# Optimization experiments

Hardware: AMD Instinct MI355X
Metric: run time of the kernel (lower is better)

The kernel has to match this reference:

```python
import jax, jax.numpy as jnp
import numpy as np
import math

NSAMPLE = 16
ATTN_TEMP = 1.0
LEAKY = 0.1
BN_EPS = 1e-5


def _knn(k, query, ref):
    # query [B,Nq,3], ref [B,Nr,3] -> idx [B,Nq,k] (indices into ref, nearest first)
    d = (jnp.sum(query * query, -1)[:, :, None]
         + jnp.sum(ref * ref, -1)[:, None, :]
         - 2.0 * jnp.einsum('bqc,brc->bqr', query, ref))
    _, idx = jax.lax.top_k(-d, k)
    return idx


def _gather(pts, idx):
    # pts [B,N,C], idx [B,M,K] -> [B,M,K,C]
    return jax.vmap(lambda p, i: p[i])(pts, idx)


def _bn_eval(x, g, b):
    # eval-mode BatchNorm2d with running_mean=0, running_var=1
    return x * (g / jnp.sqrt(1.0 + BN_EPS)) + b


def _leaky(x):
    return jnp.where(x >= 0, x, LEAKY * x)


def setup_inputs() -> dict:
    key = jax.random.key(0)
    ks = jax.random.split(key, 25)
    B, N, D, Cm, H = 2, 4096, 64, 64, 8
    f = jax.random.normal
    inp = {
        'xyz1': f(ks[0], (B, 3, N), jnp.float32),
        'xyz2': f(ks[1], (B, 3, N), jnp.float32),
        'xyz2w': f(ks[2], (B, 3, N), jnp.float32),
        'points1': f(ks[3], (B, D, N), jnp.float32),
        'points2': f(ks[4], (B, D, N), jnp.float32),
        'mlp_W0': f(ks[5], (Cm, 2 * D + 3), jnp.float32) * 0.1,
        'mlp_b0': f(ks[6], (Cm,), jnp.float32) * 0.05,
        'mlp_W1': f(ks[7], (Cm, Cm), jnp.float32) * 0.1,
        'mlp_b1': f(ks[8], (Cm,), jnp.float32) * 0.05,
        'wn_W0': f(ks[9], (H, 3), jnp.float32) * 0.3,
        'wn_b0': f(ks[10], (H,), jnp.float32) * 0.05,
        'wn_g0': jax.random.uniform(ks[11], (H,), jnp.float32, 0.5, 1.5),
        'wn_be0': f(ks[12], (H,), jnp.float32) * 0.05,
        'wn_W1': f(ks[13], (H, H), jnp.float32) * 0.3,
        'wn_b1': f(ks[14], (H,), jnp.float32) * 0.05,
        'wn_g1': jax.random.uniform(ks[15], (H,), jnp.float32, 0.5, 1.5),
        'wn_be1': f(ks[16], (H,), jnp.float32) * 0.05,
        'wn_W2': f(ks[17], (Cm, H), jnp.float32) * 0.3,
        'wn_b2': f(ks[18], (Cm,), jnp.float32) * 0.05,
        'wn_g2': jax.random.uniform(ks[19], (Cm,), jnp.float32, 0.5, 1.5),
        'wn_be2': f(ks[20], (Cm,), jnp.float32) * 0.05,
    }
    return inp


def reference(xyz1, xyz2, xyz2w, points1, points2,
              mlp_W0, mlp_b0, mlp_W1, mlp_b1,
              wn_W0, wn_b0, wn_g0, wn_be0,
              wn_W1, wn_b1, wn_g1, wn_be1,
              wn_W2, wn_b2, wn_g2, wn_be2):
    K = NSAMPLE
    B, C, N1 = xyz1.shape  # C == 3
    p1 = xyz1.transpose(0, 2, 1)    # [B,N1,3]
    p2 = xyz2.transpose(0, 2, 1)
    p2w = xyz2w.transpose(0, 2, 1)
    f1 = points1.transpose(0, 2, 1)  # [B,N1,D]
    f2 = points2.transpose(0, 2, 1)

    def mlp(f):
        f = _leaky(jnp.einsum('bnkc,oc->bnko', f, mlp_W0) + mlp_b0)
        f = _leaky(jnp.einsum('bnkc,oc->bnko', f, mlp_W1) + mlp_b1)
        return f

    idx = _knn(K, p1, p2)
    dir_xyz = _gather(p2, idx) - p1[:, :, None, :]          # [B,N1,K,3]
    idxw = _knn(K, p1, p2w)
    dir_xyzw = _gather(p2w, idxw) - p1[:, :, None, :]

    g1 = jnp.broadcast_to(f1[:, :, None, :], (B, N1, K, f1.shape[-1]))
    feat = mlp(jnp.concatenate([g1, _gather(f2, idx), dir_xyz], -1))    # [B,N1,K,Cm]
    featw = mlp(jnp.concatenate([g1, _gather(f2, idxw), dir_xyzw], -1))  # [B,N1,K,Cm]

    # per-channel K x K attention, contracted over all N1 points
    wqk = jnp.einsum('bnkc,bnlc->bckl', feat, featw)        # [B,Cm,K,K]
    wqk = jnp.clip(jax.nn.softmax(wqk / ATTN_TEMP, -1) / math.sqrt(C), 1e-10)
    # sum over trailing K is pushed into the attention matrix (same math)
    costw = jnp.einsum('bnlc,bcl->bcn', featw, wqk.sum(-1))  # [B,Cm,N1]
    cost = jnp.einsum('bnlc,bcl->bcn', feat, wqk.sum(-2))    # [B,Cm,N1]

    # self-neighborhood aggregation with WeightNet (bn=True, eval mode)
    idx_s = _knn(K, p1, p1)
    dir_s = _gather(p1, idx_s) - p1[:, :, None, :]           # [B,N1,K,3]
    h = jax.nn.relu(_bn_eval(jnp.einsum('bnkc,oc->bnko', dir_s, wn_W0) + wn_b0, wn_g0, wn_be0))
    h = jax.nn.relu(_bn_eval(jnp.einsum('bnkc,oc->bnko', h, wn_W1) + wn_b1, wn_g1, wn_be1))
    w = jax.nn.relu(_bn_eval(jnp.einsum('bnkc,oc->bnko', h, wn_W2) + wn_b2, wn_g2, wn_be2))  # [B,N1,K,Cm]

    grouped = _gather(cost.transpose(0, 2, 1), idx_s) + _gather(costw.transpose(0, 2, 1), idx_s)  # [B,N1,K,Cm]
    return jnp.einsum('bnkc,bnkc->bcn', w, grouped)          # [B,Cm,N1]
```

## Files before the change

### kernel.cpp

```cpp
#include <hip/hip_runtime.h>
#include <math.h>

#define B_  2
#define N_  4096
#define K_  16
#define D_  64
#define CM_ 64
#define H_  8

#define NSEG  8
#define SEGSZ (N_ / NSEG)
#define QPB   256
#define LIM   16
#define BATCH 8
#define TAUS  512

__device__ __forceinline__ void ce64(unsigned long long& a, unsigned long long& b) {
    bool sw = b < a;
    unsigned long long lo = sw ? b : a;
    unsigned long long hi = sw ? a : b;
    a = lo; b = hi;
}
__device__ __forceinline__ void cef(float& a, float& b) {
    float lo = fminf(a, b), hi = fmaxf(a, b);
    a = lo; b = hi;
}

#define SORT16_(e, CE) do { \
    CE(e[0],e[1]); CE(e[2],e[3]); CE(e[4],e[5]); CE(e[6],e[7]); \
    CE(e[8],e[9]); CE(e[10],e[11]); CE(e[12],e[13]); CE(e[14],e[15]); \
    CE(e[0],e[2]); CE(e[1],e[3]); CE(e[4],e[6]); CE(e[5],e[7]); \
    CE(e[8],e[10]); CE(e[9],e[11]); CE(e[12],e[14]); CE(e[13],e[15]); \
    CE(e[1],e[2]); CE(e[5],e[6]); CE(e[9],e[10]); CE(e[13],e[14]); \
    CE(e[0],e[4]); CE(e[1],e[5]); CE(e[2],e[6]); CE(e[3],e[7]); \
    CE(e[8],e[12]); CE(e[9],e[13]); CE(e[10],e[14]); CE(e[11],e[15]); \
    CE(e[2],e[4]); CE(e[3],e[5]); CE(e[10],e[12]); CE(e[11],e[13]); \
    CE(e[1],e[2]); CE(e[3],e[4]); CE(e[5],e[6]); \
    CE(e[9],e[10]); CE(e[11],e[12]); CE(e[13],e[14]); \
    CE(e[0],e[8]); CE(e[1],e[9]); CE(e[2],e[10]); CE(e[3],e[11]); \
    CE(e[4],e[12]); CE(e[5],e[13]); CE(e[6],e[14]); CE(e[7],e[15]); \
    CE(e[4],e[8]); CE(e[5],e[9]); CE(e[6],e[10]); CE(e[7],e[11]); \
    CE(e[2],e[4]); CE(e[3],e[5]); CE(e[6],e[8]); CE(e[7],e[9]); \
    CE(e[10],e[12]); CE(e[11],e[13]); \
    CE(e[1],e[2]); CE(e[3],e[4]); CE(e[5],e[6]); CE(e[7],e[8]); \
    CE(e[9],e[10]); CE(e[11],e[12]); CE(e[13],e[14]); \
} while (0)

#define BMERGE16_(d, CE) do { \
    CE(d[0],d[8]); CE(d[1],d[9]); CE(d[2],d[10]); CE(d[3],d[11]); \
    CE(d[4],d[12]); CE(d[5],d[13]); CE(d[6],d[14]); CE(d[7],d[15]); \
    CE(d[0],d[4]); CE(d[1],d[5]); CE(d[2],d[6]); CE(d[3],d[7]); \
    CE(d[8],d[12]); CE(d[9],d[13]); CE(d[10],d[14]); CE(d[11],d[15]); \
    CE(d[0],d[2]); CE(d[1],d[3]); CE(d[4],d[6]); CE(d[5],d[7]); \
    CE(d[8],d[10]); CE(d[9],d[11]); CE(d[12],d[14]); CE(d[13],d[15]); \
    CE(d[0],d[1]); CE(d[2],d[3]); CE(d[4],d[5]); CE(d[6],d[7]); \
    CE(d[8],d[9]); CE(d[10],d[11]); CE(d[12],d[13]); CE(d[14],d[15]); \
} while (0)

__global__ __launch_bounds__(256) void knn_tau_kernel(
    const float* __restrict__ xyz1, const float* __restrict__ xyz2,
    const float* __restrict__ xyz2w,
    float* __restrict__ tauBuf)
{
    const int b = blockIdx.y, which = blockIdx.z;
    const float* q = xyz1 + (size_t)b * 3 * N_;
    const float* r = (which == 0 ? xyz2 : (which == 1 ? xyz2w : xyz1)) + (size_t)b * 3 * N_;

    const int tid = threadIdx.x;
    const int qi = blockIdx.x * QPB + tid;
    const float qx = q[qi], qy = q[N_ + qi], qz = q[2 * N_ + qi];
    const float qq = qx * qx + qy * qy + qz * qz;

    __shared__ float4 tile[TAUS];
    __shared__ float  bufD[LIM * QPB];

    float bd[K_];
#pragma unroll
    for (int i = 0; i < K_; ++i) bd[i] = 3.4e38f;
    float tau = 3.4e38f;
    float c = 0.5f * (qq - tau);
    c -= fabsf(c) * 0.0009765625f + 1e-20f;
    int cnt = 0;

    for (int j = tid; j < TAUS; j += QPB) {
        float x = r[j], y = r[N_ + j], z = r[2 * N_ + j];
        tile[j] = make_float4(x, y, z, x * x + y * y + z * z);
    }
    __syncthreads();

    auto compactF = [&](int m_end) {
        float e[16];
#pragma unroll
        for (int m = 0; m < 16; ++m) {
            float dv = bufD[m * QPB + tid];
            e[m] = (m < m_end) ? dv : 3.4e38f;
        }
        SORT16_(e, cef);
#pragma unroll
        for (int i = 0; i < 16; ++i) bd[i] = fminf(bd[i], e[15 - i]);
        BMERGE16_(bd, cef);
        tau = fminf(tau, bd[K_ - 1]);
        c = 0.5f * (qq - tau);
        c -= fabsf(c) * 0.0009765625f + 1e-20f;
    };

    for (int j0 = 0; j0 < TAUS; j0 += BATCH) {
        float s8[BATCH], d8[BATCH];
#pragma unroll
        for (int u = 0; u < BATCH; ++u) {
            float4 t = tile[j0 + u];
            float dot = qx * t.x + qy * t.y + qz * t.z;
            s8[u] = dot - 0.5f * t.w;
            d8[u] = fmaxf((qq + t.w) - 2.0f * dot, 0.0f);
        }
#pragma unroll
        for (int u = 0; u < BATCH; ++u) {
            if (s8[u] > c) { bufD[cnt * QPB + tid] = d8[u]; ++cnt; }
        }
        if (__any(cnt > 8)) { compactF(cnt); cnt = 0; }
    }
    if (__any(cnt != 0)) compactF(cnt);

    tauBuf[((size_t)b * 3 + which) * N_ + qi] = bd[K_ - 1];
}

__global__ __launch_bounds__(256) void knn_seg_kernel(
    const float* __restrict__ xyz1, const float* __restrict__ xyz2,
    const float* __restrict__ xyz2w,
    const float* __restrict__ tauBuf,
    float* __restrict__ segD, int* __restrict__ segI)
{
    const int b = blockIdx.y;
    const int which = blockIdx.z >> 3;
    const int seg   = blockIdx.z & 7;
    const float* q = xyz1 + (size_t)b * 3 * N_;
    const float* r = (which == 0 ? xyz2 : (which == 1 ? xyz2w : xyz1)) + (size_t)b * 3 * N_;

    const int tid = threadIdx.x;
    const int qi = blockIdx.x * QPB + tid;
    const float qx = q[qi], qy = q[N_ + qi], qz = q[2 * N_ + qi];
    const float qq = qx * qx + qy * qy + qz * qz;

    __shared__ float4 tile[SEGSZ];
    __shared__ float  bufD[LIM * QPB];
    __shared__ int    bufI[LIM * QPB];

    unsigned long long bd[K_];
#pragma unroll
    for (int i = 0; i < K_; ++i) bd[i] = ~0ull;
    float tau = tauBuf[((size_t)b * 3 + which) * N_ + qi];
    float c = 0.5f * (qq - tau);
    c -= fabsf(c) * 0.0009765625f + 1e-20f;
    int cnt = 0;

    const int base0 = seg * SEGSZ;
    for (int j = tid; j < SEGSZ; j += QPB) {
        float x = r[base0 + j], y = r[N_ + base0 + j], z = r[2 * N_ + base0 + j];
        tile[j] = make_float4(x, y, z, x * x + y * y + z * z);
    }
    __syncthreads();

    auto compact = [&](int m_end) {
        unsigned long long e[16];
#pragma unroll
        for (int m = 0; m < 16; ++m) {
            float dv = bufD[m * QPB + tid];
            int   iv = bufI[m * QPB + tid];
            unsigned long long key =
                ((unsigned long long)__float_as_uint(dv) << 32) | (unsigned)iv;
            e[m] = (m < m_end) ? key : ~0ull;
        }
        SORT16_(e, ce64);
#pragma unroll
        for (int i = 0; i < 16; ++i) {
            unsigned long long cand = e[15 - i];
            if (cand < bd[i]) bd[i] = cand;
        }
        BMERGE16_(bd, ce64);
        tau = fminf(tau, __uint_as_float((unsigned)(bd[K_ - 1] >> 32)));
        c = 0.5f * (qq - tau);
        c -= fabsf(c) * 0.0009765625f + 1e-20f;
    };

    for (int j0 = 0; j0 < SEGSZ; j0 += BATCH) {
        float s8[BATCH], d8[BATCH];
#pragma unroll
        for (int u = 0; u < BATCH; ++u) {
            float4 t = tile[j0 + u];
            float dot = qx * t.x + qy * t.y + qz * t.z;
            s8[u] = dot - 0.5f * t.w;
            d8[u] = fmaxf((qq + t.w) - 2.0f * dot, 0.0f);
        }
#pragma unroll
        for (int u = 0; u < BATCH; ++u) {
            if (s8[u] > c) {
                bufD[cnt * QPB + tid] = d8[u];
                bufI[cnt * QPB + tid] = base0 + j0 + u;
                ++cnt;
            }
        }
        if (__any(cnt > 8)) { compact(cnt); cnt = 0; }
    }
    if (__any(cnt != 0)) compact(cnt);

    const size_t ob = ((((size_t)b * 3 + which) * NSEG + seg) * N_ + qi) * K_;
#pragma unroll
    for (int i = 0; i < K_; ++i) {
        segD[ob + i] = __uint_as_float((unsigned)(bd[i] >> 32));
        segI[ob + i] = (int)(unsigned)bd[i];
    }
}

__global__ __launch_bounds__(256) void knn_merge_kernel(
    const float* __restrict__ segD, const int* __restrict__ segI,
    int* __restrict__ idxA, int* __restrict__ idxB, int* __restrict__ idxS)
{
    const int b = blockIdx.y, which = blockIdx.z;
    const int qi = blockIdx.x * 256 + threadIdx.x;
    unsigned long long m[K_];
#pragma unroll
    for (int i = 0; i < K_; ++i) m[i] = ~0ull;
    for (int s = 0; s < NSEG; ++s) {
        const size_t ob = ((((size_t)b * 3 + which) * NSEG + s) * N_ + qi) * K_;
        for (int e = 0; e < K_; ++e) {
            unsigned long long key =
                ((unsigned long long)__float_as_uint(segD[ob + e]) << 32)
                | (unsigned)segI[ob + e];
            if (key >= m[K_ - 1]) break;
            m[K_ - 1] = key;
#pragma unroll
            for (int i = K_ - 1; i > 0; --i) {
                if (m[i] < m[i - 1]) {
                    unsigned long long t = m[i]; m[i] = m[i - 1]; m[i - 1] = t;
                }
            }
        }
    }
    int* outp = (which == 0 ? idxA : (which == 1 ? idxB : idxS));
    int* op = outp + ((size_t)b * N_ + qi) * K_;
#pragma unroll
    for (int i = 0; i < K_; ++i) op[i] = (int)(unsigned)m[i];
}

__global__ __launch_bounds__(256) void pre_gemm_kernel(
    const float* __restrict__ points1, const float* __restrict__ points2,
    const float* __restrict__ W0,
    float* __restrict__ G1, float* __restrict__ P2)
{
    const int b = blockIdx.y, which = blockIdx.z;
    const float* src = which ? points2 : points1;
    float* dst = which ? P2 : G1;
    const int woff = which ? 64 : 0;
    const int n0 = blockIdx.x * 64;
    const int tid = threadIdx.x;

    __shared__ float sW[64 * 65];
    __shared__ float sA[64 * 68];

    for (int i = tid; i < 4096; i += 256) {
        int c = i & 63, o = i >> 6;
        sW[c * 65 + o] = W0[o * 131 + woff + c];
    }
    for (int i = tid; i < 4096; i += 256) {
        int n = i & 63, c = i >> 6;
        sA[c * 68 + n] = src[((size_t)b * 64 + c) * N_ + n0 + n];
    }
    __syncthreads();

    const int o = tid & 63, qg = tid >> 6;
    float acc[16];
#pragma unroll
    for (int j = 0; j < 16; ++j) acc[j] = 0.f;
    for (int c = 0; c < 64; ++c) {
        float w = sW[c * 65 + o];
        const float4* ap = (const float4*)&sA[c * 68 + qg * 16];
#pragma unroll
        for (int m = 0; m < 4; ++m) {
            float4 a4 = ap[m];
            acc[4 * m + 0] += w * a4.x;
            acc[4 * m + 1] += w * a4.y;
            acc[4 * m + 2] += w * a4.z;
            acc[4 * m + 3] += w * a4.w;
        }
    }
#pragma unroll
    for (int j = 0; j < 16; ++j)
        dst[((size_t)b * N_ + n0 + qg * 16 + j) * 64 + o] = acc[j];
}

__global__ __launch_bounds__(256) void mlp2_kernel(
    const float* __restrict__ xyz1, const float* __restrict__ xyz2,
    const float* __restrict__ xyz2w,
    const int* __restrict__ idxA, const int* __restrict__ idxB,
    const float* __restrict__ G1, const float* __restrict__ P2,
    const float* __restrict__ W0, const float* __restrict__ b0,
    const float* __restrict__ W1, const float* __restrict__ b1,
    float* __restrict__ feat, float* __restrict__ featw)
{
    const int b = blockIdx.y, which = blockIdx.z;
    const int* idx = which ? idxB : idxA;
    const float* refxyz = (which ? xyz2w : xyz2) + (size_t)b * 3 * N_;
    float* outp = which ? featw : feat;
    const int n0 = blockIdx.x * 8;
    const int tid = threadIdx.x;
    const int w = tid >> 6, lane = tid & 63;

    __shared__ float sh0[64 * 132];
    __shared__ float sW1[64 * 68];
    __shared__ float sWc[3 * 64];
    __shared__ float sB0[64];
    __shared__ float sQ[3][8];
    __shared__ int   sIdx[128];

    for (int i = tid; i < 4096; i += 256) {
        int c = i & 63, o = i >> 6;
        sW1[c * 68 + o] = W1[o * 64 + c];
    }
    if (tid < 192) { int m = tid >> 6, o = tid & 63; sWc[m * 64 + o] = W0[o * 131 + 128 + m]; }
    if (tid < 64) sB0[tid] = b0[tid];
    if (tid < 24) { int m = tid >> 3, j = tid & 7; sQ[m][j] = xyz1[((size_t)b * 3 + m) * N_ + n0 + j]; }
    if (tid < 128) sIdx[tid] = idx[((size_t)b * N_ + n0 + (tid >> 4)) * K_ + (tid & 15)];
    __syncthreads();

    {
        const int o = lane;
        const float wc0 = sWc[o], wc1 = sWc[64 + o], wc2 = sWc[128 + o];
        const float bb0 = sB0[o];
#pragma unroll
        for (int p = 0; p < 2; ++p) {
            const int pl = w * 2 + p;
            const float g1 = G1[((size_t)b * N_ + n0 + pl) * 64 + o];
            const float qx = sQ[0][pl], qy = sQ[1][pl], qz = sQ[2][pl];
            for (int k = 0; k < K_; ++k) {
                const int row = pl * K_ + k;
                const int ii = sIdx[row];
                float p2 = P2[((size_t)b * N_ + ii) * 64 + o];
                float dx = refxyz[ii] - qx;
                float dy = refxyz[N_ + ii] - qy;
                float dz = refxyz[2 * N_ + ii] - qz;
                float h = g1 + p2 + dx * wc0 + dy * wc1 + dz * wc2 + bb0;
                h = h >= 0.f ? h : 0.1f * h;
                sh0[o * 132 + row] = h;
            }
        }
    }
    __syncthreads();

    const int lr = lane >> 3, lo = lane & 7;
    float accv[4][8];
    {
        float4 bva = *(const float4*)&b1[lo * 8];
        float4 bvb = *(const float4*)&b1[lo * 8 + 4];
#pragma unroll
        for (int dr = 0; dr < 4; ++dr) {
            accv[dr][0] = bva.x; accv[dr][1] = bva.y; accv[dr][2] = bva.z; accv[dr][3] = bva.w;
            accv[dr][4] = bvb.x; accv[dr][5] = bvb.y; accv[dr][6] = bvb.z; accv[dr][7] = bvb.w;
        }
    }
    for (int c = 0; c < 64; ++c) {
        float4 a4 = *(const float4*)&sh0[c * 132 + w * 32 + lr * 4];
        float4 wa = *(const float4*)&sW1[c * 68 + lo * 8];
        float4 wb = *(const float4*)&sW1[c * 68 + lo * 8 + 4];
        float av[4] = {a4.x, a4.y, a4.z, a4.w};
        float wv[8] = {wa.x, wa.y, wa.z, wa.w, wb.x, wb.y, wb.z, wb.w};
#pragma unroll
        for (int dr = 0; dr < 4; ++dr)
#pragma unroll
            for (int j = 0; j < 8; ++j)
                accv[dr][j] += av[dr] * wv[j];
    }
#pragma unroll
    for (int dr = 0; dr < 4; ++dr) {
        const int row = w * 32 + lr * 4 + dr;
        const int pl = row >> 4, k = row & 15;
        float o8[8];
#pragma unroll
        for (int j = 0; j < 8; ++j) {
            float v = accv[dr][j];
            o8[j] = v >= 0.f ? v : 0.1f * v;
        }
        float* op = outp + (((size_t)b * N_ + n0 + pl) * K_ + k) * 64 + lo * 8;
        *(float4*)op = make_float4(o8[0], o8[1], o8[2], o8[3]);
        *(float4*)(op + 4) = make_float4(o8[4], o8[5], o8[6], o8[7]);
    }
}

#define NCHUNK 32
#define CG 16

__global__ __launch_bounds__(256) void attn_partial_kernel(
    const float* __restrict__ feat, const float* __restrict__ featw,
    float* __restrict__ partial)
{
    const int chunk = blockIdx.x;
    const int b = blockIdx.y >> 2;
    const int c0 = (blockIdx.y & 3) * CG;
    const int tid = threadIdx.x;
    const int k = tid >> 4, c = tid & 15;

    __shared__ float sf[16 * 16 * 17];
    __shared__ float sfw[16 * 16 * 20];

    float acc[K_];
#pragma unroll
    for (int l = 0; l < K_; ++l) acc[l] = 0.f;

    const int n0 = chunk * (N_ / NCHUNK);
    for (int ns = 0; ns < N_ / NCHUNK; ns += 16) {
        __syncthreads();
        for (int i = tid; i < 4096; i += 256) {
            int nn = i >> 8, p = (i >> 4) & 15, qv = i & 15;
            size_t base = (((size_t)b * N_ + n0 + ns + nn) * K_ + p) * CM_ + c0 + qv;
            sf[nn * 272 + p * 17 + qv]  = feat[base];
            sfw[nn * 320 + qv * 20 + p] = featw[base];
        }
        __syncthreads();
#pragma unroll
        for (int nn = 0; nn < 16; ++nn) {
            float f = sf[nn * 272 + k * 17 + c];
            const float4* fp = (const float4*)&sfw[nn * 320 + c * 20];
#pragma unroll
            for (int m = 0; m < 4; ++m) {
                float4 v = fp[m];
                acc[4 * m + 0] += f * v.x;
                acc[4 * m + 1] += f * v.y;
                acc[4 * m + 2] += f * v.z;
                acc[4 * m + 3] += f * v.w;
            }
        }
    }
    float* pp = partial + ((((size_t)b * NCHUNK + chunk) * CM_ + (c0 + c)) * K_ + k) * K_;
#pragma unroll
    for (int m = 0; m < 4; ++m)
        *(float4*)(pp + 4 * m) = make_float4(acc[4 * m], acc[4 * m + 1], acc[4 * m + 2], acc[4 * m + 3]);
}

__global__ __launch_bounds__(256) void attn_reduce_kernel(
    const float* __restrict__ partial,
    float* __restrict__ rowsum, float* __restrict__ colsum)
{
    const int c = blockIdx.x, b = blockIdx.y;
    const int tid = threadIdx.x;
    const int k = tid >> 4, l = tid & 15;
    __shared__ float smat[K_][K_ + 1];

    float acc = 0.f;
#pragma unroll
    for (int ch = 0; ch < NCHUNK; ++ch)
        acc += partial[((((size_t)b * NCHUNK + ch) * CM_ + c) * K_ + k) * K_ + l];

    float m = acc;
#pragma unroll
    for (int off = 8; off >= 1; off >>= 1) m = fmaxf(m, __shfl_xor(m, off, 16));
    float e = expf(acc - m);
    float s = e;
#pragma unroll
    for (int off = 8; off >= 1; off >>= 1) s += __shfl_xor(s, off, 16);
    float sm = fmaxf((e / s) * 0.57735026918962576f, 1e-10f);

    float rs = sm;
#pragma unroll
    for (int off = 8; off >= 1; off >>= 1) rs += __shfl_xor(rs, off, 16);
    if (l == 0) rowsum[((size_t)b * CM_ + c) * K_ + k] = rs;

    smat[k][l] = sm;
    __syncthreads();
    if (tid < K_) {
        float cs = 0.f;
#pragma unroll
        for (int kk = 0; kk < K_; ++kk) cs += smat[kk][tid];
        colsum[((size_t)b * CM_ + c) * K_ + tid] = cs;
    }
}

__global__ __launch_bounds__(256) void cost_kernel(
    const float* __restrict__ feat, const float* __restrict__ featw,
    const float* __restrict__ rowsum, const float* __restrict__ colsum,
    float* __restrict__ costT, float* __restrict__ costwT)
{
    const int b = blockIdx.y;
    const int tid = threadIdx.x;
    __shared__ float scs[64][K_ + 1], srs[64][K_ + 1];
    for (int i = tid; i < 64 * K_; i += 256) {
        int cc = i >> 4, j = i & 15;
        scs[cc][j] = colsum[((size_t)b * CM_ + cc) * K_ + j];
        srs[cc][j] = rowsum[((size_t)b * CM_ + cc) * K_ + j];
    }
    __syncthreads();
    const int ng = tid >> 6, c = tid & 63;
    const int n = blockIdx.x * 4 + ng;
    const float* fp  = feat  + (((size_t)b * N_ + n) * K_) * 64 + c;
    const float* fwp = featw + (((size_t)b * N_ + n) * K_) * 64 + c;
    float a = 0.f, aw = 0.f;
#pragma unroll
    for (int j = 0; j < K_; ++j) {
        a  += fp[j * 64]  * scs[c][j];
        aw += fwp[j * 64] * srs[c][j];
    }
    costT[((size_t)b * N_ + n) * 64 + c]  = a;
    costwT[((size_t)b * N_ + n) * 64 + c] = aw;
}

__global__ __launch_bounds__(256) void final_kernel(
    const float* __restrict__ xyz1,
    const int* __restrict__ idxS,
    const float* __restrict__ costT, const float* __restrict__ costwT,
    const float* __restrict__ wn_W0, const float* __restrict__ wn_b0,
    const float* __restrict__ wn_g0, const float* __restrict__ wn_be0,
    const float* __restrict__ wn_W1, const float* __restrict__ wn_b1,
    const float* __restrict__ wn_g1, const float* __restrict__ wn_be1,
    const float* __restrict__ wn_W2, const float* __restrict__ wn_b2,
    const float* __restrict__ wn_g2, const float* __restrict__ wn_be2,
    float* __restrict__ out)
{
    const int b = blockIdx.y;
    const int tid = threadIdx.x;
    const int ng = tid >> 6, c = tid & 63;
    const int n = blockIdx.x * 4 + ng;
    const float invs = 1.0f / sqrtf(1.0f + 1e-5f);

    __shared__ int   sI[4][K_];
    __shared__ float sH1[4][K_][H_];

    if (c < K_) {
        const int k = c;
        const float* qb = xyz1 + (size_t)b * 3 * N_;
        int ii = idxS[((size_t)b * N_ + n) * K_ + k];
        sI[ng][k] = ii;
        float dx = qb[ii] - qb[n];
        float dy = qb[N_ + ii] - qb[N_ + n];
        float dz = qb[2 * N_ + ii] - qb[2 * N_ + n];
        float h0[H_];
#pragma unroll
        for (int o = 0; o < H_; ++o) {
            float v = wn_W0[o * 3] * dx + wn_W0[o * 3 + 1] * dy + wn_W0[o * 3 + 2] * dz + wn_b0[o];
            v = v * (wn_g0[o] * invs) + wn_be0[o];
            h0[o] = fmaxf(v, 0.f);
        }
#pragma unroll
        for (int o = 0; o < H_; ++o) {
            float v = wn_b1[o];
#pragma unroll
            for (int j = 0; j < H_; ++j) v += wn_W1[o * H_ + j] * h0[j];
            v = v * (wn_g1[o] * invs) + wn_be1[o];
            sH1[ng][k][o] = fmaxf(v, 0.f);
        }
    }
    __syncthreads();

    float w2r[H_];
#pragma unroll
    for (int j = 0; j < H_; ++j) w2r[j] = wn_W2[c * H_ + j];
    const float b2v = wn_b2[c];
    const float s2v = wn_g2[c] * invs;
    const float t2v = wn_be2[c];

    float acc = 0.f;
#pragma unroll
    for (int k = 0; k < K_; ++k) {
        float v = b2v;
#pragma unroll
        for (int j = 0; j < H_; ++j) v += w2r[j] * sH1[ng][k][j];
        float wv = fmaxf(v * s2v + t2v, 0.f);
        int ii = sI[ng][k];
        size_t base = ((size_t)b * N_ + ii) * 64 + c;
        acc += wv * (costT[base] + costwT[base]);
    }
    out[((size_t)b * CM_ + c) * N_ + n] = acc;
}

extern "C" void kernel_launch(void* const* d_in, const int* in_sizes, int n_in,
                              void* d_out, int out_size, void* d_ws, size_t ws_size,
                              hipStream_t stream)
{
    const float* xyz1    = (const float*)d_in[0];
    const float* xyz2    = (const float*)d_in[1];
    const float* xyz2w   = (const float*)d_in[2];
    const float* points1 = (const float*)d_in[3];
    const float* points2 = (const float*)d_in[4];
    const float* mlp_W0  = (const float*)d_in[5];
    const float* mlp_b0  = (const float*)d_in[6];
    const float* mlp_W1  = (const float*)d_in[7];
    const float* mlp_b1  = (const float*)d_in[8];
    const float* wn_W0   = (const float*)d_in[9];
    const float* wn_b0   = (const float*)d_in[10];
    const float* wn_g0   = (const float*)d_in[11];
    const float* wn_be0  = (const float*)d_in[12];
    const float* wn_W1   = (const float*)d_in[13];
    const float* wn_b1   = (const float*)d_in[14];
    const float* wn_g1   = (const float*)d_in[15];
    const float* wn_be1  = (const float*)d_in[16];
    const float* wn_W2   = (const float*)d_in[17];
    const float* wn_b2   = (const float*)d_in[18];
    const float* wn_g2   = (const float*)d_in[19];
    const float* wn_be2  = (const float*)d_in[20];
    float* out = (float*)d_out;

    char* ws = (char*)d_ws;
    size_t off = 0;
    auto alloc = [&](size_t bytes) -> void* {
        void* p = ws + off;
        off += (bytes + 255) & ~(size_t)255;
        return p;
    };
    int*   idxA   = (int*)  alloc((size_t)B_ * N_ * K_ * sizeof(int));
    int*   idxB   = (int*)  alloc((size_t)B_ * N_ * K_ * sizeof(int));
    int*   idxS   = (int*)  alloc((size_t)B_ * N_ * K_ * sizeof(int));
    float* tauBuf = (float*)alloc((size_t)B_ * 3 * N_ * sizeof(float));
    float* feat   = (float*)alloc((size_t)B_ * N_ * K_ * CM_ * sizeof(float));
    float* featw  = (float*)alloc((size_t)B_ * N_ * K_ * CM_ * sizeof(float));
    float* rowsum = (float*)alloc((size_t)B_ * CM_ * K_ * sizeof(float));
    float* colsum = (float*)alloc((size_t)B_ * CM_ * K_ * sizeof(float));
    float* costT  = (float*)alloc((size_t)B_ * N_ * CM_ * sizeof(float));
    float* costwT = (float*)alloc((size_t)B_ * N_ * CM_ * sizeof(float));
    (void)ws_size; (void)in_sizes; (void)n_in; (void)out_size;

    float* segD    = feat;
    int*   segI    = (int*)featw;
    float* G1      = costT;
    float* P2      = costwT;
    float* partial = costT;

    pre_gemm_kernel<<<dim3(N_ / 64, B_, 2), 256, 0, stream>>>(points1, points2, mlp_W0, G1, P2);
    knn_tau_kernel<<<dim3(N_ / QPB, B_, 3), QPB, 0, stream>>>(
        xyz1, xyz2, xyz2w, tauBuf);
    knn_seg_kernel<<<dim3(N_ / QPB, B_, 3 * NSEG), QPB, 0, stream>>>(
        xyz1, xyz2, xyz2w, tauBuf, segD, segI);
    knn_merge_kernel<<<dim3(N_ / 256, B_, 3), 256, 0, stream>>>(
        segD, segI, idxA, idxB, idxS);
    mlp2_kernel<<<dim3(N_ / 8, B_, 2), 256, 0, stream>>>(
        xyz1, xyz2, xyz2w, idxA, idxB, G1, P2,
        mlp_W0, mlp_b0, mlp_W1, mlp_b1, feat, featw);
    attn_partial_kernel<<<dim3(NCHUNK, 4 * B_), 256, 0, stream>>>(feat, featw, partial);
    attn_reduce_kernel<<<dim3(CM_, B_), 256, 0, stream>>>(partial, rowsum, colsum);
    cost_kernel<<<dim3(N_ / 4, B_), 256, 0, stream>>>(feat, featw, rowsum, colsum, costT, costwT);
    final_kernel<<<dim3(N_ / 4, B_), 256, 0, stream>>>(xyz1, idxS, costT, costwT,
                                                       wn_W0, wn_b0, wn_g0, wn_be0,
                                                       wn_W1, wn_b1, wn_g1, wn_be1,
                                                       wn_W2, wn_b2, wn_g2, wn_be2, out);
}
```

Baseline: 253.6 us.

## Defer distance computation in KNN candidate buffers, transpose seg layout, prefetch attn tiles

The KNN tau and segment kernels now run a lighter filter pass. It computes one fused score per reference point and writes candidates branchlessly, storing only a score (tau kernel) or a local index (seg kernel). Full distances are recomputed from the shared tile inside the compaction step, which removes the separate distance buffer and the divergent stores. The segment outputs are transposed to a K-major, query-contiguous layout so the merge reads are coalesced. The attention partial kernel prefetches the next global tile into registers while computing on the current one, at the cost of extra registers.

```diff
diff --git a/kernel.cpp b/kernel.cpp
--- a/kernel.cpp
+++ b/kernel.cpp
@@ -72,7 +72,7 @@
     const float qq = qx * qx + qy * qy + qz * qz;
 
     __shared__ float4 tile[TAUS];
-    __shared__ float  bufD[LIM * QPB];
+    __shared__ float  bufS[LIM * QPB];
 
     float bd[K_];
 #pragma unroll
@@ -84,7 +84,7 @@
 
     for (int j = tid; j < TAUS; j += QPB) {
         float x = r[j], y = r[N_ + j], z = r[2 * N_ + j];
-        tile[j] = make_float4(x, y, z, x * x + y * y + z * z);
+        tile[j] = make_float4(x, y, z, -0.5f * (x * x + y * y + z * z));
     }
     __syncthreads();
 
@@ -92,7 +92,8 @@
         float e[16];
 #pragma unroll
         for (int m = 0; m < 16; ++m) {
-            float dv = bufD[m * QPB + tid];
+            float sv = bufS[m * QPB + tid];
+            float dv = fmaxf(qq - 2.0f * sv, 0.0f);
             e[m] = (m < m_end) ? dv : 3.4e38f;
         }
         SORT16_(e, cef);
@@ -105,17 +106,16 @@
     };
 
     for (int j0 = 0; j0 < TAUS; j0 += BATCH) {
-        float s8[BATCH], d8[BATCH];
+        float s8[BATCH];
 #pragma unroll
         for (int u = 0; u < BATCH; ++u) {
             float4 t = tile[j0 + u];
-            float dot = qx * t.x + qy * t.y + qz * t.z;
-            s8[u] = dot - 0.5f * t.w;
-            d8[u] = fmaxf((qq + t.w) - 2.0f * dot, 0.0f);
+            s8[u] = qx * t.x + (qy * t.y + (qz * t.z + t.w));
         }
 #pragma unroll
         for (int u = 0; u < BATCH; ++u) {
-            if (s8[u] > c) { bufD[cnt * QPB + tid] = d8[u]; ++cnt; }
+            bufS[cnt * QPB + tid] = s8[u];
+            cnt += (s8[u] > c) ? 1 : 0;
         }
         if (__any(cnt > 8)) { compactF(cnt); cnt = 0; }
     }
@@ -142,7 +142,6 @@
     const float qq = qx * qx + qy * qy + qz * qz;
 
     __shared__ float4 tile[SEGSZ];
-    __shared__ float  bufD[LIM * QPB];
     __shared__ int    bufI[LIM * QPB];
 
     unsigned long long bd[K_];
@@ -156,7 +155,7 @@
     const int base0 = seg * SEGSZ;
     for (int j = tid; j < SEGSZ; j += QPB) {
         float x = r[base0 + j], y = r[N_ + base0 + j], z = r[2 * N_ + base0 + j];
-        tile[j] = make_float4(x, y, z, x * x + y * y + z * z);
+        tile[j] = make_float4(x, y, z, -0.5f * (x * x + y * y + z * z));
     }
     __syncthreads();
 
@@ -164,10 +163,14 @@
         unsigned long long e[16];
 #pragma unroll
         for (int m = 0; m < 16; ++m) {
-            float dv = bufD[m * QPB + tid];
-            int   iv = bufI[m * QPB + tid];
+            int j = bufI[m * QPB + tid] & (SEGSZ - 1);
+            float4 t = tile[j];
+            float dot = qx * t.x + qy * t.y + qz * t.z;
+            float rr = -2.0f * t.w;
+            float dv = fmaxf((qq + rr) - 2.0f * dot, 0.0f);
             unsigned long long key =
-                ((unsigned long long)__float_as_uint(dv) << 32) | (unsigned)iv;
+                ((unsigned long long)__float_as_uint(dv) << 32)
+                | (unsigned)(base0 + j);
             e[m] = (m < m_end) ? key : ~0ull;
         }
         SORT16_(e, ce64);
@@ -183,31 +186,26 @@
     };
 
     for (int j0 = 0; j0 < SEGSZ; j0 += BATCH) {
-        float s8[BATCH], d8[BATCH];
+        float s8[BATCH];
 #pragma unroll
         for (int u = 0; u < BATCH; ++u) {
             float4 t = tile[j0 + u];
-            float dot = qx * t.x + qy * t.y + qz * t.z;
-            s8[u] = dot - 0.5f * t.w;
-            d8[u] = fmaxf((qq + t.w) - 2.0f * dot, 0.0f);
+            s8[u] = qx * t.x + (qy * t.y + (qz * t.z + t.w));
         }
 #pragma unroll
         for (int u = 0; u < BATCH; ++u) {
-            if (s8[u] > c) {
-                bufD[cnt * QPB + tid] = d8[u];
-                bufI[cnt * QPB + tid] = base0 + j0 + u;
-                ++cnt;
-            }
+            bufI[cnt * QPB + tid] = j0 + u;
+            cnt += (s8[u] > c) ? 1 : 0;
         }
         if (__any(cnt > 8)) { compact(cnt); cnt = 0; }
     }
     if (__any(cnt != 0)) compact(cnt);
 
-    const size_t ob = ((((size_t)b * 3 + which) * NSEG + seg) * N_ + qi) * K_;
+    const size_t ob = (((size_t)(b * 3 + which) * NSEG + seg) * K_) * N_ + qi;
 #pragma unroll
     for (int i = 0; i < K_; ++i) {
-        segD[ob + i] = __uint_as_float((unsigned)(bd[i] >> 32));
-        segI[ob + i] = (int)(unsigned)bd[i];
+        segD[ob + (size_t)i * N_] = __uint_as_float((unsigned)(bd[i] >> 32));
+        segI[ob + (size_t)i * N_] = (int)(unsigned)bd[i];
     }
 }
 
@@ -221,11 +219,11 @@
 #pragma unroll
     for (int i = 0; i < K_; ++i) m[i] = ~0ull;
     for (int s = 0; s < NSEG; ++s) {
-        const size_t ob = ((((size_t)b * 3 + which) * NSEG + s) * N_ + qi) * K_;
+        const size_t ob = (((size_t)(b * 3 + which) * NSEG + s) * K_) * N_ + qi;
         for (int e = 0; e < K_; ++e) {
             unsigned long long key =
-                ((unsigned long long)__float_as_uint(segD[ob + e]) << 32)
-                | (unsigned)segI[ob + e];
+                ((unsigned long long)__float_as_uint(segD[ob + (size_t)e * N_]) << 32)
+                | (unsigned)segI[ob + (size_t)e * N_];
             if (key >= m[K_ - 1]) break;
             m[K_ - 1] = key;
 #pragma unroll
@@ -387,6 +385,7 @@
 
 #define NCHUNK 32
 #define CG 16
+#define NITER ((N_ / NCHUNK) / 16)
 
 __global__ __launch_bounds__(256) void attn_partial_kernel(
     const float* __restrict__ feat, const float* __restrict__ featw,
@@ -406,15 +405,34 @@
     for (int l = 0; l < K_; ++l) acc[l] = 0.f;
 
     const int n0 = chunk * (N_ / NCHUNK);
-    for (int ns = 0; ns < N_ / NCHUNK; ns += 16) {
-        __syncthreads();
-        for (int i = tid; i < 4096; i += 256) {
+    float rf[16], rfw[16];
+
+    auto LOADG = [&](int ns) {
+#pragma unroll
+        for (int t = 0; t < 16; ++t) {
+            int i = tid + t * 256;
             int nn = i >> 8, p = (i >> 4) & 15, qv = i & 15;
             size_t base = (((size_t)b * N_ + n0 + ns + nn) * K_ + p) * CM_ + c0 + qv;
-            sf[nn * 272 + p * 17 + qv]  = feat[base];
-            sfw[nn * 320 + qv * 20 + p] = featw[base];
-        }
+            rf[t]  = feat[base];
+            rfw[t] = featw[base];
+        }
+    };
+    auto STORE = [&]() {
+#pragma unroll
+        for (int t = 0; t < 16; ++t) {
+            int i = tid + t * 256;
+            int nn = i >> 8, p = (i >> 4) & 15, qv = i & 15;
+            sf[nn * 272 + p * 17 + qv]  = rf[t];
+            sfw[nn * 320 + qv * 20 + p] = rfw[t];
+        }
+    };
+
+    LOADG(0);
+    for (int it = 0; it < NITER; ++it) {
         __syncthreads();
+        STORE();
+        __syncthreads();
+        if (it + 1 < NITER) LOADG((it + 1) * 16);
 #pragma unroll
         for (int nn = 0; nn < 16; ++nn) {
             float f = sf[nn * 272 + k * 17 + c];
```

After: 238.5 us. -5.9%, faster.
